# Performance work log

Hardware: AMD Instinct MI355X
Metric: run time of the kernel (lower is better)

The kernel has to match this reference:

```python
import jax, jax.numpy as jnp
import numpy as np

N = 100000      # nodes
E = 1600000     # edges (before self-loops)
IN_C = 128
HID = 256
L = 4
EPS = 1e-5


def setup_inputs() -> dict:
    key = jax.random.key(0)
    ks = jax.random.split(key, 12)
    s = 0.05
    x = jax.random.normal(ks[0], (N, IN_C), dtype=jnp.float32)
    edge_index = jax.random.randint(ks[1], (2, E), 0, N, dtype=jnp.int64)
    enc_w = jax.random.normal(ks[2], (IN_C, HID), dtype=jnp.float32) * s
    enc_b = jnp.zeros((HID,), jnp.float32)
    conv_w = jax.random.normal(ks[3], (L, HID, HID), dtype=jnp.float32) * s
    conv_b = jnp.zeros((L, HID), jnp.float32)
    ln_g = jnp.ones((L, HID), jnp.float32)
    ln_b = jnp.zeros((L, HID), jnp.float32)
    lin1_w = jax.random.normal(ks[4], (HID, HID // 2), dtype=jnp.float32) * s
    lin1_b = jnp.zeros((HID // 2,), jnp.float32)
    lin2_w = jax.random.normal(ks[5], (HID // 2, 1), dtype=jnp.float32) * s
    lin2_b = jnp.zeros((1,), jnp.float32)
    return dict(x=x, edge_index=edge_index, enc_w=enc_w, enc_b=enc_b,
                conv_w=conv_w, conv_b=conv_b, ln_g=ln_g, ln_b=ln_b,
                lin1_w=lin1_w, lin1_b=lin1_b, lin2_w=lin2_w, lin2_b=lin2_b)


def _layer_norm(h, g, b):
    mu = jnp.mean(h, axis=-1, keepdims=True)
    var = jnp.mean(jnp.square(h - mu), axis=-1, keepdims=True)
    return (h - mu) * jax.lax.rsqrt(var + EPS) * g + b


def reference(x, edge_index, enc_w, enc_b, conv_w, conv_b, ln_g, ln_b,
              lin1_w, lin1_b, lin2_w, lin2_b):
    loops = jnp.arange(N, dtype=edge_index.dtype)
    row = jnp.concatenate([edge_index[0], loops])   # source
    col = jnp.concatenate([edge_index[1], loops])   # target
    # GCN symmetric norm with self-loop weight 1 (improved=False)
    deg = jax.ops.segment_sum(jnp.ones(row.shape[0], jnp.float32), col,
                              num_segments=N)
    dis = jnp.where(deg > 0, jax.lax.rsqrt(deg), 0.0)  # deg^-1/2, [N]

    h = x @ enc_w + enc_b
    for i in range(L):
        hw = h @ conv_w[i]
        # norm_e = dis[row]*dis[col]: scale at source, aggregate, scale at target
        agg = jax.ops.segment_sum((hw * dis[:, None])[row], col,
                                  num_segments=N)
        h = agg * dis[:, None] + conv_b[i]
        h = jax.nn.relu(_layer_norm(h, ln_g[i], ln_b[i]))
        # dropout p=0.1 is identity in eval mode
    h = jax.nn.relu(h @ lin1_w + lin1_b)
    return h @ lin2_w + lin2_b  # [N, 1]
```

## Files before the change

kernel.cpp:

```cpp
#include <hip/hip_runtime.h>

#define N_NODES 100000
#define N_EDGES 1600000
#define IN_C    128
#define HID     256
#define NLAYER  4

#define NBUCK 391
#define BCAP  8192
#define EPB   4096
#define CAPL  6144

typedef __attribute__((ext_vector_type(8))) __bf16 bf16x8;
typedef __attribute__((ext_vector_type(4))) float  floatx4;

__device__ inline unsigned short f2b(float f) {
    unsigned u = __builtin_bit_cast(unsigned, f);
    return (unsigned short)((u + 0x7fffu + ((u >> 16) & 1u)) >> 16);
}
__device__ inline float b2f(unsigned short s) {
    unsigned u = ((unsigned)s) << 16;
    return __builtin_bit_cast(float, u);
}
__device__ inline void acc8(float* a, uint4 v) {
    unsigned wds[4] = {v.x, v.y, v.z, v.w};
    #pragma unroll
    for (int k = 0; k < 4; ++k) {
        a[2*k]   += __builtin_bit_cast(float, wds[k] << 16);
        a[2*k+1] += __builtin_bit_cast(float, wds[k] & 0xffff0000u);
    }
}

__global__ void kb_zero(int* g, int m) {
    int i = blockIdx.x * blockDim.x + threadIdx.x;
    if (i < m) g[i] = 0;
}

__global__ __launch_bounds__(256) void kb_scatter(
        const int* __restrict__ row, const int* __restrict__ col,
        int* __restrict__ gfill, uint2* __restrict__ pairs, int e) {
    __shared__ uint2 ep[EPB];
    __shared__ int hist[NBUCK];
    __shared__ int lbase[NBUCK];
    const int tid  = threadIdx.x;
    const int base = blockIdx.x * EPB;
    for (int b = tid; b < NBUCK; b += 256) hist[b] = 0;
    __syncthreads();
    #pragma unroll
    for (int k = 0; k < EPB / 256; ++k) {
        int i = base + k * 256 + tid;
        uint2 pr = make_uint2(0xffffffffu, 0u);
        if (i < e) {
            pr.x = (unsigned)col[i];
            pr.y = (unsigned)row[i];
            atomicAdd(&hist[pr.x >> 8], 1);
        }
        ep[k * 256 + tid] = pr;
    }
    __syncthreads();
    for (int b = tid; b < NBUCK; b += 256) {
        int h = hist[b];
        lbase[b] = h ? atomicAdd(&gfill[b], h) : 0;
    }
    __syncthreads();
    for (int b = tid; b < NBUCK; b += 256) hist[b] = 0;
    __syncthreads();
    #pragma unroll
    for (int k = 0; k < EPB / 256; ++k) {
        uint2 pr = ep[k * 256 + tid];
        if (pr.x != 0xffffffffu) {
            int bk = pr.x >> 8;
            int p  = lbase[bk] + atomicAdd(&hist[bk], 1);
            if (p < BCAP) pairs[(size_t)bk * BCAP + p] = pr;
        }
    }
}

__global__ void kb_scan(const int* __restrict__ gfill, int* __restrict__ boff,
                        int* __restrict__ offs) {
    __shared__ int wsum[8];
    const int t = threadIdx.x, lane = t & 63, w = t >> 6;
    int v = (t < NBUCK) ? gfill[t] : 0;
    int inc = v;
    #pragma unroll
    for (int o = 1; o < 64; o <<= 1) { int u = __shfl_up(inc, o); if (lane >= o) inc += u; }
    if (lane == 63) wsum[w] = inc;
    __syncthreads();
    if (t == 0) { int r = 0; for (int i = 0; i < 8; ++i) { int x = wsum[i]; wsum[i] = r; r += x; } }
    __syncthreads();
    int excl = wsum[w] + inc - v;
    if (t <= NBUCK) boff[t] = excl;
    if (t == 0) offs[N_NODES] = N_EDGES;
}

__global__ __launch_bounds__(256) void kb_build(
        const uint2* __restrict__ pairs, const int* __restrict__ gfill,
        const int* __restrict__ boff,
        int* __restrict__ offs, float* __restrict__ dis,
        int* __restrict__ srcl, int n) {
    __shared__ int lcnt[256];
    __shared__ int lstart[256];
    __shared__ int wsum[4];
    __shared__ int sl[CAPL];
    const int b = blockIdx.x;
    const int tid = threadIdx.x, lane = tid & 63, w = tid >> 6;
    int cnt = gfill[b]; if (cnt > CAPL) cnt = CAPL;
    const int base = boff[b];
    const uint2* bp = pairs + (size_t)b * BCAP;
    lcnt[tid] = 0;
    __syncthreads();
    for (int i = tid; i < cnt; i += 256)
        atomicAdd(&lcnt[bp[i].x & 255], 1);
    __syncthreads();
    int v = lcnt[tid];
    int inc = v;
    #pragma unroll
    for (int o = 1; o < 64; o <<= 1) { int u = __shfl_up(inc, o); if (lane >= o) inc += u; }
    if (lane == 63) wsum[w] = inc;
    __syncthreads();
    if (tid == 0) { int r = 0; for (int i = 0; i < 4; ++i) { int x = wsum[i]; wsum[i] = r; r += x; } }
    __syncthreads();
    int excl = wsum[w] + inc - v;
    lstart[tid] = excl;
    int node = (b << 8) + tid;
    if (node < n) {
        dis[node]  = rsqrtf((float)(v + 1));
        offs[node] = base + excl;
    }
    __syncthreads();
    lcnt[tid] = 0;
    __syncthreads();
    for (int i = tid; i < cnt; i += 256) {
        uint2 pr = bp[i];
        int c = pr.x & 255;
        int q = lstart[c] + atomicAdd(&lcnt[c], 1);
        sl[q] = (int)pr.y;
    }
    __syncthreads();
    for (int i = tid; i < cnt; i += 256)
        srcl[base + i] = sl[i];
}

__global__ void k_f2b4(const float* __restrict__ src, unsigned short* __restrict__ dst, int n4) {
    int i = blockIdx.x * blockDim.x + threadIdx.x;
    if (i < n4) {
        float4 v = ((const float4*)src)[i];
        ushort4 o;
        o.x = f2b(v.x); o.y = f2b(v.y); o.z = f2b(v.z); o.w = f2b(v.w);
        ((ushort4*)dst)[i] = o;
    }
}

__global__ void k_wt(const float* __restrict__ W, unsigned short* __restrict__ Wt, int K, int Nn) {
    int idx = blockIdx.x * blockDim.x + threadIdx.x;
    if (idx < K * Nn) {
        int k = idx / Nn, n = idx % Nn;
        Wt[n * K + k] = f2b(W[idx]);
    }
}

template<int MODE>
__global__ __launch_bounds__(256) void k_mm(
        const unsigned short* __restrict__ A,
        const unsigned short* __restrict__ Wt,
        const float* __restrict__ bias, const float* __restrict__ scale,
        void* __restrict__ Cout, int M, int K, int Nn) {
    __shared__ unsigned short As[128 * 32];
    __shared__ unsigned short Bs[128 * 32];
    const int tid  = threadIdx.x;
    const int lane = tid & 63;
    const int w    = tid >> 6;
    const int bm   = blockIdx.x * 128;
    const int bn   = blockIdx.y * 128;

    const int i0 = tid, i1 = tid + 256;
    const int r0 = i0 >> 2, r1 = i1 >> 2;
    const int q0 = i0 & 3,  q1 = i1 & 3;
    const int a_off0 = min(bm + r0, M - 1) * K + q0 * 8;
    const int a_off1 = min(bm + r1, M - 1) * K + q1 * 8;
    const int b_off0 = (bn + r0) * K + q0 * 8;
    const int b_off1 = (bn + r1) * K + q1 * 8;

    uint4 ra0, ra1, rb0, rb1;
    floatx4 acc[4][4];
    #pragma unroll
    for (int i = 0; i < 4; ++i)
        #pragma unroll
        for (int j = 0; j < 4; ++j)
            acc[i][j] = (floatx4){0.f, 0.f, 0.f, 0.f};

    const int wm = (w & 1) * 64;
    const int wn = (w >> 1) * 64;
    const int fm = lane & 15;
    const int fq = (lane >> 4) * 8;

    ra0 = *(const uint4*)(A  + a_off0);
    ra1 = *(const uint4*)(A  + a_off1);
    rb0 = *(const uint4*)(Wt + b_off0);
    rb1 = *(const uint4*)(Wt + b_off1);

    const int KT = K >> 5;
    for (int kt = 0; kt < KT; ++kt) {
        ((uint4*)As)[i0] = ra0; ((uint4*)As)[i1] = ra1;
        ((uint4*)Bs)[i0] = rb0; ((uint4*)Bs)[i1] = rb1;
        __syncthreads();
        if (kt + 1 < KT) {
            int k0 = (kt + 1) << 5;
            ra0 = *(const uint4*)(A  + a_off0 + k0);
            ra1 = *(const uint4*)(A  + a_off1 + k0);
            rb0 = *(const uint4*)(Wt + b_off0 + k0);
            rb1 = *(const uint4*)(Wt + b_off1 + k0);
        }
        bf16x8 af[4], bfr[4];
        #pragma unroll
        for (int i = 0; i < 4; ++i)
            af[i] = *(const bf16x8*)(const void*)(As + (wm + i * 16 + fm) * 32 + fq);
        #pragma unroll
        for (int j = 0; j < 4; ++j)
            bfr[j] = *(const bf16x8*)(const void*)(Bs + (wn + j * 16 + fm) * 32 + fq);
        #pragma unroll
        for (int i = 0; i < 4; ++i)
            #pragma unroll
            for (int j = 0; j < 4; ++j)
                acc[i][j] = __builtin_amdgcn_mfma_f32_16x16x32_bf16(af[i], bfr[j], acc[i][j], 0, 0, 0);
        __syncthreads();
    }

    const int quad = lane >> 4;
    #pragma unroll
    for (int i = 0; i < 4; ++i) {
        #pragma unroll
        for (int r = 0; r < 4; ++r) {
            int row = bm + wm + i * 16 + quad * 4 + r;
            if (row >= M) continue;
            float sc = scale ? scale[row] : 1.f;
            #pragma unroll
            for (int j = 0; j < 4; ++j) {
                int colg = bn + wn + j * 16 + fm;
                float v = acc[i][j][r];
                if (MODE == 0) v += bias[colg];
                v *= sc;
                ((unsigned short*)Cout)[(size_t)row * Nn + colg] = f2b(v);
            }
        }
    }
}

__global__ __launch_bounds__(256) void k_head(
        const unsigned short* __restrict__ A,
        const unsigned short* __restrict__ Wt,
        const float* __restrict__ b1, const float* __restrict__ w2,
        const float* __restrict__ b2, float* __restrict__ out, int M) {
    const int K = 256;
    __shared__ unsigned short As[128 * 32];
    __shared__ unsigned short Bs[128 * 32];
    const int tid  = threadIdx.x;
    const int lane = tid & 63;
    const int w    = tid >> 6;
    const int bm   = blockIdx.x * 128;

    const int i0 = tid, i1 = tid + 256;
    const int r0 = i0 >> 2, r1 = i1 >> 2;
    const int q0 = i0 & 3,  q1 = i1 & 3;
    const int a_off0 = min(bm + r0, M - 1) * K + q0 * 8;
    const int a_off1 = min(bm + r1, M - 1) * K + q1 * 8;
    const int b_off0 = r0 * K + q0 * 8;
    const int b_off1 = r1 * K + q1 * 8;

    uint4 ra0, ra1, rb0, rb1;
    floatx4 acc[4][4];
    #pragma unroll
    for (int i = 0; i < 4; ++i)
        #pragma unroll
        for (int j = 0; j < 4; ++j)
            acc[i][j] = (floatx4){0.f, 0.f, 0.f, 0.f};

    const int wm = (w & 1) * 64;
    const int wn = (w >> 1) * 64;
    const int fm = lane & 15;
    const int fq = (lane >> 4) * 8;

    ra0 = *(const uint4*)(A  + a_off0);
    ra1 = *(const uint4*)(A  + a_off1);
    rb0 = *(const uint4*)(Wt + b_off0);
    rb1 = *(const uint4*)(Wt + b_off1);

    for (int kt = 0; kt < 8; ++kt) {
        ((uint4*)As)[i0] = ra0; ((uint4*)As)[i1] = ra1;
        ((uint4*)Bs)[i0] = rb0; ((uint4*)Bs)[i1] = rb1;
        __syncthreads();
        if (kt + 1 < 8) {
            int k0 = (kt + 1) << 5;
            ra0 = *(const uint4*)(A  + a_off0 + k0);
            ra1 = *(const uint4*)(A  + a_off1 + k0);
            rb0 = *(const uint4*)(Wt + b_off0 + k0);
            rb1 = *(const uint4*)(Wt + b_off1 + k0);
        }
        bf16x8 af[4], bfr[4];
        #pragma unroll
        for (int i = 0; i < 4; ++i)
            af[i] = *(const bf16x8*)(const void*)(As + (wm + i * 16 + fm) * 32 + fq);
        #pragma unroll
        for (int j = 0; j < 4; ++j)
            bfr[j] = *(const bf16x8*)(const void*)(Bs + (wn + j * 16 + fm) * 32 + fq);
        #pragma unroll
        for (int i = 0; i < 4; ++i)
            #pragma unroll
            for (int j = 0; j < 4; ++j)
                acc[i][j] = __builtin_amdgcn_mfma_f32_16x16x32_bf16(af[i], bfr[j], acc[i][j], 0, 0, 0);
        __syncthreads();
    }

    float* red = (float*)As;
    const int q = lane >> 4;
    float b1v[4], w2v[4];
    #pragma unroll
    for (int j = 0; j < 4; ++j) {
        int col = wn + j * 16 + fm;
        b1v[j] = b1[col]; w2v[j] = w2[col];
    }
    #pragma unroll
    for (int i = 0; i < 4; ++i) {
        #pragma unroll
        for (int r = 0; r < 4; ++r) {
            float s = 0.f;
            #pragma unroll
            for (int j = 0; j < 4; ++j)
                s += fmaxf(acc[i][j][r] + b1v[j], 0.f) * w2v[j];
            #pragma unroll
            for (int off = 1; off < 16; off <<= 1) s += __shfl_xor(s, off);
            if (fm == 0) {
                int m = wm + i * 16 + q * 4 + r;
                red[m * 2 + (wn >> 6)] = s;
            }
        }
    }
    __syncthreads();
    if (tid < 128) {
        int row = bm + tid;
        if (row < M) out[row] = red[tid * 2] + red[tid * 2 + 1] + b2[0];
    }
}

__global__ void k_agg(const unsigned short* __restrict__ hw, const int* __restrict__ srcl,
                      const int* __restrict__ offs, const float* __restrict__ dis,
                      const float* __restrict__ cb, const float* __restrict__ g,
                      const float* __restrict__ bt, unsigned short* __restrict__ hout, int n) {
    int gtid = blockIdx.x * blockDim.x + threadIdx.x;
    int node = __builtin_amdgcn_readfirstlane(gtid >> 6);
    int lane = threadIdx.x & 63;
    const int half = lane >> 5;
    const int sub  = lane & 31;
    const uint4* T = (const uint4*)hw;

    float a[8] = {0,0,0,0,0,0,0,0};
    float c[8] = {0,0,0,0,0,0,0,0};
    if (half == 0) {
        uint4 v = T[(size_t)node * 32 + sub];
        acc8(a, v);
    }
    int p = offs[node], pe = offs[node + 1];
    for (; p + 7 < pe; p += 8) {
        int s0 = srcl[p],     s1 = srcl[p + 1], s2 = srcl[p + 2], s3 = srcl[p + 3];
        int s4 = srcl[p + 4], s5 = srcl[p + 5], s6 = srcl[p + 6], s7 = srcl[p + 7];
        int ea = half ? s1 : s0;
        int eb = half ? s3 : s2;
        int ec = half ? s5 : s4;
        int ed = half ? s7 : s6;
        uint4 va = T[(size_t)ea * 32 + sub];
        uint4 vb = T[(size_t)eb * 32 + sub];
        uint4 vc = T[(size_t)ec * 32 + sub];
        uint4 vd = T[(size_t)ed * 32 + sub];
        acc8(a, va);
        acc8(c, vb);
        acc8(a, vc);
        acc8(c, vd);
    }
    for (; p + 1 < pe; p += 2) {
        int s0 = srcl[p], s1 = srcl[p + 1];
        int ea = half ? s1 : s0;
        uint4 v = T[(size_t)ea * 32 + sub];
        acc8(a, v);
    }
    if (p < pe && half == 0) {
        int s0 = srcl[p];
        uint4 v = T[(size_t)s0 * 32 + sub];
        acc8(a, v);
    }
    #pragma unroll
    for (int j = 0; j < 8; ++j) {
        a[j] += c[j];
        a[j] += __shfl_xor(a[j], 32);
    }
    float dc = dis[node];
    const float4* cb4 = (const float4*)cb;
    const float4* g4  = (const float4*)g;
    const float4* bt4 = (const float4*)bt;
    float4 cba = cb4[sub * 2], cbb = cb4[sub * 2 + 1];
    float h[8];
    h[0] = fmaf(a[0], dc, cba.x); h[1] = fmaf(a[1], dc, cba.y);
    h[2] = fmaf(a[2], dc, cba.z); h[3] = fmaf(a[3], dc, cba.w);
    h[4] = fmaf(a[4], dc, cbb.x); h[5] = fmaf(a[5], dc, cbb.y);
    h[6] = fmaf(a[6], dc, cbb.z); h[7] = fmaf(a[7], dc, cbb.w);
    float s = 0.f, sq = 0.f;
    #pragma unroll
    for (int j = 0; j < 8; ++j) { s += h[j]; sq += h[j] * h[j]; }
    #pragma unroll
    for (int off = 1; off < 32; off <<= 1) { s += __shfl_xor(s, off); sq += __shfl_xor(sq, off); }
    float mu  = s * (1.f / 256.f);
    float var = sq * (1.f / 256.f) - mu * mu;
    float inv = rsqrtf(var + 1e-5f);
    if (half == 0) {
        float4 ga = g4[sub * 2], gb = g4[sub * 2 + 1];
        float4 ba = bt4[sub * 2], bb = bt4[sub * 2 + 1];
        float gv[8] = {ga.x, ga.y, ga.z, ga.w, gb.x, gb.y, gb.z, gb.w};
        float bv[8] = {ba.x, ba.y, ba.z, ba.w, bb.x, bb.y, bb.z, bb.w};
        unsigned short o[8];
        #pragma unroll
        for (int j = 0; j < 8; ++j)
            o[j] = f2b(fmaxf(fmaf((h[j] - mu) * inv, gv[j], bv[j]), 0.f));
        uint4 st;
        st.x = (unsigned)o[0] | ((unsigned)o[1] << 16);
        st.y = (unsigned)o[2] | ((unsigned)o[3] << 16);
        st.z = (unsigned)o[4] | ((unsigned)o[5] << 16);
        st.w = (unsigned)o[6] | ((unsigned)o[7] << 16);
        ((uint4*)hout)[(size_t)node * 32 + sub] = st;
    }
}

extern "C" void kernel_launch(void* const* d_in, const int* in_sizes, int n_in,
                              void* d_out, int out_size, void* d_ws, size_t ws_size,
                              hipStream_t stream) {
    const float* x      = (const float*)d_in[0];
    const int*   ei     = (const int*)d_in[1];
    const float* enc_w  = (const float*)d_in[2];
    const float* enc_b  = (const float*)d_in[3];
    const float* conv_w = (const float*)d_in[4];
    const float* conv_b = (const float*)d_in[5];
    const float* ln_g   = (const float*)d_in[6];
    const float* ln_b   = (const float*)d_in[7];
    const float* w1     = (const float*)d_in[8];
    const float* b1     = (const float*)d_in[9];
    const float* w2     = (const float*)d_in[10];
    const float* b2     = (const float*)d_in[11];
    float* out = (float*)d_out;

    char* ws = (char*)d_ws;
    size_t off = 0;
    auto alloc = [&](size_t bytes) -> void* {
        void* p = ws + off;
        off = (off + bytes + 255) & ~(size_t)255;
        return p;
    };
    int*   offs  = (int*)alloc((size_t)(N_NODES + 1) * 4);
    int*   srcl  = (int*)alloc((size_t)N_EDGES * 4);
    float* dis   = (float*)alloc((size_t)N_NODES * 4);
    int*   gfill = (int*)alloc((size_t)NBUCK * 4);
    int*   boff  = (int*)alloc((size_t)(NBUCK + 1) * 4);
    unsigned short* hb = (unsigned short*)alloc((size_t)N_NODES * HID * 2);
    unsigned short* hw = (unsigned short*)alloc((size_t)N_NODES * HID * 2);
    size_t pairs_bytes = (size_t)NBUCK * BCAP * 8;
    size_t xb_bytes    = (size_t)N_NODES * IN_C * 2;
    char* R3 = (char*)alloc(pairs_bytes > xb_bytes ? pairs_bytes : xb_bytes);
    uint2*          pairs = (uint2*)R3;
    unsigned short* xb    = (unsigned short*)R3;
    unsigned short* enc_t  = (unsigned short*)alloc((size_t)IN_C * HID * 2);
    unsigned short* conv_t = (unsigned short*)alloc((size_t)NLAYER * HID * HID * 2);
    unsigned short* lin1_t = (unsigned short*)alloc((size_t)HID * (HID / 2) * 2);

    const int* row = ei;
    const int* col = ei + N_EDGES;

    kb_zero<<<(NBUCK + 255) / 256, 256, 0, stream>>>(gfill, NBUCK);
    kb_scatter<<<(N_EDGES + EPB - 1) / EPB, 256, 0, stream>>>(row, col, gfill, pairs, N_EDGES);
    kb_scan<<<1, 512, 0, stream>>>(gfill, boff, offs);
    kb_build<<<NBUCK, 256, 0, stream>>>(pairs, gfill, boff, offs, dis, srcl, N_NODES);

    int xn4 = N_NODES * IN_C / 4;
    k_f2b4<<<(xn4 + 255) / 256, 256, 0, stream>>>(x, xb, xn4);
    k_wt<<<(IN_C * HID + 255) / 256, 256, 0, stream>>>(enc_w, enc_t, IN_C, HID);
    for (int l = 0; l < NLAYER; ++l)
        k_wt<<<(HID * HID + 255) / 256, 256, 0, stream>>>(
            conv_w + (size_t)l * HID * HID, conv_t + (size_t)l * HID * HID, HID, HID);
    k_wt<<<(HID * (HID / 2) + 255) / 256, 256, 0, stream>>>(w1, lin1_t, HID, HID / 2);

    {
        dim3 g((N_NODES + 127) / 128, HID / 128);
        k_mm<0><<<g, 256, 0, stream>>>(xb, enc_t, enc_b, nullptr, hb, N_NODES, IN_C, HID);
    }

    for (int l = 0; l < NLAYER; ++l) {
        dim3 g((N_NODES + 127) / 128, HID / 128);
        k_mm<1><<<g, 256, 0, stream>>>(hb, conv_t + (size_t)l * HID * HID, nullptr, dis,
                                       hw, N_NODES, HID, HID);
        k_agg<<<(N_NODES * 64 + 255) / 256, 256, 0, stream>>>(
            hw, srcl, offs, dis, conv_b + l * HID, ln_g + l * HID, ln_b + l * HID, hb, N_NODES);
    }

    k_head<<<(N_NODES + 127) / 128, 256, 0, stream>>>(hb, lin1_t, b1, w2, b2, out, N_NODES);
}
```

Measured before the change: 833.2 us.

## Fuse input bf16 cast into encoder GEMM, merge weight prep, use direct-to-LDS loads

Folds the fp32-to-bf16 conversion of x into the encoder GEMM's A-tile load, which removes a separate cast kernel and its intermediate buffer round-trip. All weight transposes and the bucket counter zeroing are merged into one launch, cutting several tiny kernel launches. The conv and head GEMMs switch from register-staged prefetch to global_load_lds direct copies into shared memory. In exchange, those GEMMs lose their software prefetch overlap, so each K-step now waits on its own loads.

Result: faster. 803.6 us (-3.5%).

```diff
diff --git a/kernel.cpp b/kernel.cpp
--- a/kernel.cpp
+++ b/kernel.cpp
@@ -18,10 +18,6 @@
     unsigned u = __builtin_bit_cast(unsigned, f);
     return (unsigned short)((u + 0x7fffu + ((u >> 16) & 1u)) >> 16);
 }
-__device__ inline float b2f(unsigned short s) {
-    unsigned u = ((unsigned)s) << 16;
-    return __builtin_bit_cast(float, u);
-}
 __device__ inline void acc8(float* a, uint4 v) {
     unsigned wds[4] = {v.x, v.y, v.z, v.w};
     #pragma unroll
@@ -30,10 +26,10 @@
         a[2*k+1] += __builtin_bit_cast(float, wds[k] & 0xffff0000u);
     }
 }
-
-__global__ void kb_zero(int* g, int m) {
-    int i = blockIdx.x * blockDim.x + threadIdx.x;
-    if (i < m) g[i] = 0;
+__device__ inline void gl16(const void* g, void* l) {
+    __builtin_amdgcn_global_load_lds(
+        (const __attribute__((address_space(1))) unsigned int*)g,
+        (__attribute__((address_space(3))) unsigned int*)l, 16, 0, 0);
 }
 
 __global__ __launch_bounds__(256) void kb_scatter(
@@ -141,30 +137,34 @@
         srcl[base + i] = sl[i];
 }
 
-__global__ void k_f2b4(const float* __restrict__ src, unsigned short* __restrict__ dst, int n4) {
-    int i = blockIdx.x * blockDim.x + threadIdx.x;
-    if (i < n4) {
-        float4 v = ((const float4*)src)[i];
-        ushort4 o;
-        o.x = f2b(v.x); o.y = f2b(v.y); o.z = f2b(v.z); o.w = f2b(v.w);
-        ((ushort4*)dst)[i] = o;
-    }
-}
-
-__global__ void k_wt(const float* __restrict__ W, unsigned short* __restrict__ Wt, int K, int Nn) {
+__global__ void k_wtz(const float* __restrict__ enc_w, const float* __restrict__ conv_w,
+                      const float* __restrict__ w1,
+                      unsigned short* __restrict__ enc_t, unsigned short* __restrict__ conv_t,
+                      unsigned short* __restrict__ lin1_t, int* __restrict__ gfill) {
     int idx = blockIdx.x * blockDim.x + threadIdx.x;
-    if (idx < K * Nn) {
-        int k = idx / Nn, n = idx % Nn;
-        Wt[n * K + k] = f2b(W[idx]);
-    }
-}
-
-template<int MODE>
-__global__ __launch_bounds__(256) void k_mm(
-        const unsigned short* __restrict__ A,
+    if (idx < NBUCK) gfill[idx] = 0;
+    if (idx < IN_C * HID) {
+        int k = idx / HID, n = idx % HID;
+        enc_t[n * IN_C + k] = f2b(enc_w[idx]);
+    } else if (idx < IN_C * HID + NLAYER * HID * HID) {
+        int r = idx - IN_C * HID;
+        int l = r / (HID * HID);
+        int e = r % (HID * HID);
+        int k = e / HID, n = e % HID;
+        conv_t[(size_t)l * HID * HID + n * HID + k] = f2b(conv_w[r]);
+    } else if (idx < IN_C * HID + NLAYER * HID * HID + HID * (HID / 2)) {
+        int e = idx - (IN_C * HID + NLAYER * HID * HID);
+        int k = e / (HID / 2), n = e % (HID / 2);
+        lin1_t[n * HID + k] = f2b(w1[e]);
+    }
+}
+
+__global__ __launch_bounds__(256) void k_mme(
+        const float* __restrict__ Af,
         const unsigned short* __restrict__ Wt,
-        const float* __restrict__ bias, const float* __restrict__ scale,
-        void* __restrict__ Cout, int M, int K, int Nn) {
+        const float* __restrict__ bias,
+        unsigned short* __restrict__ Cout, int M) {
+    const int K = IN_C, Nn = HID;
     __shared__ unsigned short As[128 * 32];
     __shared__ unsigned short Bs[128 * 32];
     const int tid  = threadIdx.x;
@@ -181,7 +181,6 @@
     const int b_off0 = (bn + r0) * K + q0 * 8;
     const int b_off1 = (bn + r1) * K + q1 * 8;
 
-    uint4 ra0, ra1, rb0, rb1;
     floatx4 acc[4][4];
     #pragma unroll
     for (int i = 0; i < 4; ++i)
@@ -194,8 +193,23 @@
     const int fm = lane & 15;
     const int fq = (lane >> 4) * 8;
 
-    ra0 = *(const uint4*)(A  + a_off0);
-    ra1 = *(const uint4*)(A  + a_off1);
+    uint4 ra0, ra1, rb0, rb1;
+    auto loadA = [&](int koff, uint4& oa0, uint4& oa1) {
+        float4 f0 = *(const float4*)(Af + a_off0 + koff);
+        float4 f1 = *(const float4*)(Af + a_off0 + koff + 4);
+        oa0.x = (unsigned)f2b(f0.x) | ((unsigned)f2b(f0.y) << 16);
+        oa0.y = (unsigned)f2b(f0.z) | ((unsigned)f2b(f0.w) << 16);
+        oa0.z = (unsigned)f2b(f1.x) | ((unsigned)f2b(f1.y) << 16);
+        oa0.w = (unsigned)f2b(f1.z) | ((unsigned)f2b(f1.w) << 16);
+        float4 g0 = *(const float4*)(Af + a_off1 + koff);
+        float4 g1 = *(const float4*)(Af + a_off1 + koff + 4);
+        oa1.x = (unsigned)f2b(g0.x) | ((unsigned)f2b(g0.y) << 16);
+        oa1.y = (unsigned)f2b(g0.z) | ((unsigned)f2b(g0.w) << 16);
+        oa1.z = (unsigned)f2b(g1.x) | ((unsigned)f2b(g1.y) << 16);
+        oa1.w = (unsigned)f2b(g1.z) | ((unsigned)f2b(g1.w) << 16);
+    };
+
+    loadA(0, ra0, ra1);
     rb0 = *(const uint4*)(Wt + b_off0);
     rb1 = *(const uint4*)(Wt + b_off1);
 
@@ -206,8 +220,7 @@
         __syncthreads();
         if (kt + 1 < KT) {
             int k0 = (kt + 1) << 5;
-            ra0 = *(const uint4*)(A  + a_off0 + k0);
-            ra1 = *(const uint4*)(A  + a_off1 + k0);
+            loadA(k0, ra0, ra1);
             rb0 = *(const uint4*)(Wt + b_off0 + k0);
             rb1 = *(const uint4*)(Wt + b_off1 + k0);
         }
@@ -233,14 +246,84 @@
         for (int r = 0; r < 4; ++r) {
             int row = bm + wm + i * 16 + quad * 4 + r;
             if (row >= M) continue;
-            float sc = scale ? scale[row] : 1.f;
             #pragma unroll
             for (int j = 0; j < 4; ++j) {
                 int colg = bn + wn + j * 16 + fm;
-                float v = acc[i][j][r];
-                if (MODE == 0) v += bias[colg];
-                v *= sc;
-                ((unsigned short*)Cout)[(size_t)row * Nn + colg] = f2b(v);
+                float v = acc[i][j][r] + bias[colg];
+                Cout[(size_t)row * Nn + colg] = f2b(v);
+            }
+        }
+    }
+}
+
+__global__ __launch_bounds__(256) void k_mmc(
+        const unsigned short* __restrict__ A,
+        const unsigned short* __restrict__ Wt,
+        const float* __restrict__ scale,
+        unsigned short* __restrict__ Cout, int M) {
+    const int K = HID, Nn = HID;
+    __shared__ unsigned short As[128 * 32];
+    __shared__ unsigned short Bs[128 * 32];
+    const int tid  = threadIdx.x;
+    const int lane = tid & 63;
+    const int w    = tid >> 6;
+    const int bm   = blockIdx.x * 128;
+    const int bn   = blockIdx.y * 128;
+
+    const int i0 = tid, i1 = tid + 256;
+    const int r0 = i0 >> 2, r1 = i1 >> 2;
+    const int q0 = i0 & 3,  q1 = i1 & 3;
+    const int a_off0 = min(bm + r0, M - 1) * K + q0 * 8;
+    const int a_off1 = min(bm + r1, M - 1) * K + q1 * 8;
+    const int b_off0 = (bn + r0) * K + q0 * 8;
+    const int b_off1 = (bn + r1) * K + q1 * 8;
+
+    floatx4 acc[4][4];
+    #pragma unroll
+    for (int i = 0; i < 4; ++i)
+        #pragma unroll
+        for (int j = 0; j < 4; ++j)
+            acc[i][j] = (floatx4){0.f, 0.f, 0.f, 0.f};
+
+    const int wm = (w & 1) * 64;
+    const int wn = (w >> 1) * 64;
+    const int fm = lane & 15;
+    const int fq = (lane >> 4) * 8;
+
+    for (int kt = 0; kt < 8; ++kt) {
+        int k0 = kt << 5;
+        gl16(A  + a_off0 + k0, As + (size_t)i0 * 8);
+        gl16(A  + a_off1 + k0, As + (size_t)i1 * 8);
+        gl16(Wt + b_off0 + k0, Bs + (size_t)i0 * 8);
+        gl16(Wt + b_off1 + k0, Bs + (size_t)i1 * 8);
+        __syncthreads();
+        bf16x8 af[4], bfr[4];
+        #pragma unroll
+        for (int i = 0; i < 4; ++i)
+            af[i] = *(const bf16x8*)(const void*)(As + (wm + i * 16 + fm) * 32 + fq);
+        #pragma unroll
+        for (int j = 0; j < 4; ++j)
+            bfr[j] = *(const bf16x8*)(const void*)(Bs + (wn + j * 16 + fm) * 32 + fq);
+        #pragma unroll
+        for (int i = 0; i < 4; ++i)
+            #pragma unroll
+            for (int j = 0; j < 4; ++j)
+                acc[i][j] = __builtin_amdgcn_mfma_f32_16x16x32_bf16(af[i], bfr[j], acc[i][j], 0, 0, 0);
+        __syncthreads();
+    }
+
+    const int quad = lane >> 4;
+    #pragma unroll
+    for (int i = 0; i < 4; ++i) {
+        #pragma unroll
+        for (int r = 0; r < 4; ++r) {
+            int row = bm + wm + i * 16 + quad * 4 + r;
+            if (row >= M) continue;
+            float sc = scale[row];
+            #pragma unroll
+            for (int j = 0; j < 4; ++j) {
+                int colg = bn + wn + j * 16 + fm;
+                Cout[(size_t)row * Nn + colg] = f2b(acc[i][j][r] * sc);
             }
         }
     }
@@ -267,7 +350,6 @@
     const int b_off0 = r0 * K + q0 * 8;
     const int b_off1 = r1 * K + q1 * 8;
 
-    uint4 ra0, ra1, rb0, rb1;
     floatx4 acc[4][4];
     #pragma unroll
     for (int i = 0; i < 4; ++i)
@@ -280,22 +362,13 @@
     const int fm = lane & 15;
     const int fq = (lane >> 4) * 8;
 
-    ra0 = *(const uint4*)(A  + a_off0);
-    ra1 = *(const uint4*)(A  + a_off1);
-    rb0 = *(const uint4*)(Wt + b_off0);
-    rb1 = *(const uint4*)(Wt + b_off1);
-
     for (int kt = 0; kt < 8; ++kt) {
-        ((uint4*)As)[i0] = ra0; ((uint4*)As)[i1] = ra1;
-        ((uint4*)Bs)[i0] = rb0; ((uint4*)Bs)[i1] = rb1;
+        int k0 = kt << 5;
+        gl16(A  + a_off0 + k0, As + (size_t)i0 * 8);
+        gl16(A  + a_off1 + k0, As + (size_t)i1 * 8);
+        gl16(Wt + b_off0 + k0, Bs + (size_t)i0 * 8);
+        gl16(Wt + b_off1 + k0, Bs + (size_t)i1 * 8);
         __syncthreads();
-        if (kt + 1 < 8) {
-            int k0 = (kt + 1) << 5;
-            ra0 = *(const uint4*)(A  + a_off0 + k0);
-            ra1 = *(const uint4*)(A  + a_off1 + k0);
-            rb0 = *(const uint4*)(Wt + b_off0 + k0);
-            rb1 = *(const uint4*)(Wt + b_off1 + k0);
-        }
         bf16x8 af[4], bfr[4];
         #pragma unroll
         for (int i = 0; i < 4; ++i)
@@ -459,11 +532,7 @@
     int*   boff  = (int*)alloc((size_t)(NBUCK + 1) * 4);
     unsigned short* hb = (unsigned short*)alloc((size_t)N_NODES * HID * 2);
     unsigned short* hw = (unsigned short*)alloc((size_t)N_NODES * HID * 2);
-    size_t pairs_bytes = (size_t)NBUCK * BCAP * 8;
-    size_t xb_bytes    = (size_t)N_NODES * IN_C * 2;
-    char* R3 = (char*)alloc(pairs_bytes > xb_bytes ? pairs_bytes : xb_bytes);
-    uint2*          pairs = (uint2*)R3;
-    unsigned short* xb    = (unsigned short*)R3;
+    uint2* pairs = (uint2*)alloc((size_t)NBUCK * BCAP * 8);
     unsigned short* enc_t  = (unsigned short*)alloc((size_t)IN_C * HID * 2);
     unsigned short* conv_t = (unsigned short*)alloc((size_t)NLAYER * HID * HID * 2);
     unsigned short* lin1_t = (unsigned short*)alloc((size_t)HID * (HID / 2) * 2);
@@ -471,28 +540,23 @@
     const int* row = ei;
     const int* col = ei + N_EDGES;
 
-    kb_zero<<<(NBUCK + 255) / 256, 256, 0, stream>>>(gfill, NBUCK);
+    {
+        int tot = IN_C * HID + NLAYER * HID * HID + HID * (HID / 2);
+        k_wtz<<<(tot + 255) / 256, 256, 0, stream>>>(enc_w, conv_w, w1,
+                                                     enc_t, conv_t, lin1_t, gfill);
+    }
     kb_scatter<<<(N_EDGES + EPB - 1) / EPB, 256, 0, stream>>>(row, col, gfill, pairs, N_EDGES);
     kb_scan<<<1, 512, 0, stream>>>(gfill, boff, offs);
     kb_build<<<NBUCK, 256, 0, stream>>>(pairs, gfill, boff, offs, dis, srcl, N_NODES);
 
-    int xn4 = N_NODES * IN_C / 4;
-    k_f2b4<<<(xn4 + 255) / 256, 256, 0, stream>>>(x, xb, xn4);
-    k_wt<<<(IN_C * HID + 255) / 256, 256, 0, stream>>>(enc_w, enc_t, IN_C, HID);
-    for (int l = 0; l < NLAYER; ++l)
-        k_wt<<<(HID * HID + 255) / 256, 256, 0, stream>>>(
-            conv_w + (size_t)l * HID * HID, conv_t + (size_t)l * HID * HID, HID, HID);
-    k_wt<<<(HID * (HID / 2) + 255) / 256, 256, 0, stream>>>(w1, lin1_t, HID, HID / 2);
-
     {
         dim3 g((N_NODES + 127) / 128, HID / 128);
-        k_mm<0><<<g, 256, 0, stream>>>(xb, enc_t, enc_b, nullptr, hb, N_NODES, IN_C, HID);
+        k_mme<<<g, 256, 0, stream>>>(x, enc_t, enc_b, hb, N_NODES);
     }
 
     for (int l = 0; l < NLAYER; ++l) {
         dim3 g((N_NODES + 127) / 128, HID / 128);
-        k_mm<1><<<g, 256, 0, stream>>>(hb, conv_t + (size_t)l * HID * HID, nullptr, dis,
-                                       hw, N_NODES, HID, HID);
+        k_mmc<<<g, 256, 0, stream>>>(hb, conv_t + (size_t)l * HID * HID, dis, hw, N_NODES);
         k_agg<<<(N_NODES * 64 + 255) / 256, 256, 0, stream>>>(
             hw, srcl, offs, dis, conv_b + l * HID, ln_g + l * HID, ln_b + l * HID, hb, N_NODES);
     }
```
